# Optimization experiments

Hardware: AMD Instinct MI355X
Metric: run time of the kernel (lower is better)

The kernel has to match this reference:

```python
import jax, jax.numpy as jnp
import numpy as np
from jax import lax

EPS_BN = 1e-5
EPS_LN = 1e-5


def setup_inputs() -> dict:
    key = jax.random.key(0)
    ks = jax.random.split(key, 10)
    B, Cin, H, W = 32, 512, 56, 56
    Cout, Cr = 128, 128 // 16  # CBAM reduction 16
    x = jax.random.normal(ks[0], (B, Cin, H, W), dtype=jnp.float32)
    w_proj = jax.random.normal(ks[1], (Cout, Cin), dtype=jnp.float32) * 0.02
    bn_g = jnp.ones((Cout,), jnp.float32)
    bn_b = jnp.zeros((Cout,), jnp.float32)
    bn_m = jax.random.normal(ks[2], (Cout,), dtype=jnp.float32) * 0.1
    bn_v = jax.random.uniform(ks[3], (Cout,), dtype=jnp.float32, minval=0.5, maxval=1.5)
    ca_w1 = jax.random.normal(ks[4], (Cr, Cout), dtype=jnp.float32) * 0.05
    ca_w2 = jax.random.normal(ks[5], (Cout, Cr), dtype=jnp.float32) * 0.05
    sa_w = jax.random.normal(ks[6], (1, 2, 7, 7), dtype=jnp.float32) * 0.05
    ln_g = jnp.ones((Cout,), jnp.float32)
    ln_b = jnp.zeros((Cout,), jnp.float32)
    return dict(x=x, w_proj=w_proj, bn_g=bn_g, bn_b=bn_b, bn_m=bn_m, bn_v=bn_v,
                ca_w1=ca_w1, ca_w2=ca_w2, sa_w=sa_w, ln_g=ln_g, ln_b=ln_b)


def _cbam(x, ca_w1, ca_w2, sa_w):
    # Channel attention: shared MLP on GAP and GMP over spatial dims
    avg = x.mean(axis=(2, 3))  # [B, C]
    mx = x.max(axis=(2, 3))    # [B, C]
    mlp = lambda p: jnp.einsum('cr,br->bc', ca_w2, jax.nn.relu(jnp.einsum('rc,bc->br', ca_w1, p)))
    ca = jax.nn.sigmoid(mlp(avg) + mlp(mx))  # [B, C]
    x = x * ca[:, :, None, None]
    # Spatial attention: channel-wise avg/max -> 7x7 conv -> sigmoid
    s = jnp.stack([x.mean(axis=1), x.max(axis=1)], axis=1)  # [B, 2, H, W]
    sa = lax.conv_general_dilated(s, sa_w, (1, 1), [(3, 3), (3, 3)],
                                  dimension_numbers=('NCHW', 'OIHW', 'NCHW'))
    return x * jax.nn.sigmoid(sa)


def reference(x, w_proj, bn_g, bn_b, bn_m, bn_v, ca_w1, ca_w2, sa_w, ln_g, ln_b):
    # 1x1 conv (no bias) as GEMM over channels
    h = jnp.einsum('bchw,oc->bohw', x, w_proj)
    # BatchNorm (inference) + SiLU
    scale = (bn_g / jnp.sqrt(bn_v + EPS_BN))[None, :, None, None]
    shift = (bn_b - bn_m * bn_g / jnp.sqrt(bn_v + EPS_BN))[None, :, None, None]
    h = h * scale + shift
    h = h * jax.nn.sigmoid(h)  # SiLU
    # CBAM with residual
    y = _cbam(h, ca_w1, ca_w2, sa_w) + h
    # GAP over spatial -> LayerNorm over channels
    y = y.mean(axis=(2, 3))  # [B, C]
    mu = y.mean(axis=-1, keepdims=True)
    var = ((y - mu) ** 2).mean(axis=-1, keepdims=True)
    return (y - mu) / jnp.sqrt(var + EPS_LN) * ln_g + ln_b
```

## Files before the change

### kernel.cpp

```cpp
#include <hip/hip_runtime.h>
#include <hip/hip_bf16.h>

typedef __bf16 bf16x8 __attribute__((ext_vector_type(8)));
typedef float f32x4 __attribute__((ext_vector_type(4)));

#define NB 32
#define CIN 512
#define COUT 128
#define NP 3136
#define WIMG 56

__device__ __forceinline__ unsigned fenc(float f) {
    unsigned u = __float_as_uint(f);
    return (u & 0x80000000u) ? ~u : (u | 0x80000000u);
}
__device__ __forceinline__ float fdec(unsigned e) {
    unsigned u = (e & 0x80000000u) ? (e ^ 0x80000000u) : ~e;
    return __uint_as_float(u);
}
__device__ __forceinline__ float bflo(unsigned u) { return __uint_as_float(u << 16); }
__device__ __forceinline__ float bfhi(unsigned u) { return __uint_as_float(u & 0xffff0000u); }

__device__ __forceinline__ unsigned cvt2_fp8(float a, float b) {
    unsigned r;
    asm volatile("v_cvt_pk_fp8_f32 %0, %1, %2" : "=&v"(r) : "v"(a), "v"(b));
    return r & 0xffffu;
}
__device__ __forceinline__ unsigned pack4_fp8(unsigned u01, unsigned u23) {
    unsigned lo = cvt2_fp8(bflo(u01), bfhi(u01));
    unsigned hi = cvt2_fp8(bflo(u23), bfhi(u23));
    return lo | (hi << 16);
}
__device__ __forceinline__ unsigned pack4_fp8f(float a, float b, float c, float d) {
    return cvt2_fp8(a, b) | (cvt2_fp8(c, d) << 16);
}
__device__ __forceinline__ float fp8_entry(int v) {
    unsigned s = (v >> 7) & 1, e = (v >> 3) & 15, m = v & 7;
    if (e) return __uint_as_float((s << 31) | ((e + 120) << 23) | (m << 20));
    float f = (float)m * 0x1p-9f;
    return s ? -f : f;
}

__device__ __forceinline__ void lds_barrier() {
    asm volatile("s_waitcnt lgkmcnt(0)" ::: "memory");
    __builtin_amdgcn_s_barrier();
    __builtin_amdgcn_sched_barrier(0);
}

__global__ __launch_bounds__(256) void k_wcvt(const float* __restrict__ wp,
                                              unsigned* __restrict__ wf8,
                                              unsigned* __restrict__ zero8k)
{
    int i = blockIdx.x * 256 + threadIdx.x;
    if (i < 2 * NB * COUT) zero8k[i] = 0u;
    float4 f = *(const float4*)(wp + i * 4);
    wf8[i] = pack4_fp8f(f.x, f.y, f.z, f.w);
}

__global__ __launch_bounds__(512, 6) void k_main(
    const float* __restrict__ x, const uchar* __restrict__ wf8,
    const float* __restrict__ bn_g, const float* __restrict__ bn_b,
    const float* __restrict__ bn_m, const float* __restrict__ bn_v,
    uchar* __restrict__ hout, float* __restrict__ sumh, unsigned* __restrict__ mxenc)
{
    __shared__ __align__(16) uchar Xs[2][64 * 128];
    __shared__ __align__(16) uchar Ws[2][128 * 128];
    __shared__ float bnss[256];
    __shared__ float redS[2][COUT];
    __shared__ float redM[2][COUT];

    const int bid  = blockIdx.x;
    const int swz  = (bid & 7) * 196 + (bid >> 3);
    const int t    = threadIdx.x;
    const int b    = swz / 49;
    const int p0   = (swz % 49) * 64;
    const int lane = t & 63;
    const int l15  = lane & 15;
    const int lg   = lane >> 4;
    const int w    = t >> 6;
    const int wm   = w >> 1;
    const int wn   = w & 1;

    if (t < COUT) {
        float sc = bn_g[t] * rsqrtf(bn_v[t] + 1e-5f);
        bnss[t]        = sc;
        bnss[t + COUT] = bn_b[t] - bn_m[t] * sc;
    }

    const int pr = t & 63;
    const int kg = t >> 6;
    const float* xb = x + ((size_t)b * CIN) * NP + p0 + pr;
    const int xbyte = pr * 128 + ((kg * 16) ^ ((pr & 7) << 4));

    const int ow = t >> 2, kq = t & 3;
    const uchar* wsrc = wf8 + ow * CIN + kq * 32;
    const int wbyte0 = ow * 128 + ((kq * 32) ^ ((ow & 7) << 4));
    const int wbyte1 = ow * 128 + ((kq * 32 + 16) ^ ((ow & 7) << 4));

    f32x4 acc[2][2];
#pragma unroll
    for (int mf = 0; mf < 2; ++mf)
#pragma unroll
        for (int nf = 0; nf < 2; ++nf) acc[mf][nf] = (f32x4){0.f, 0.f, 0.f, 0.f};

    float ldx[2][16];
    uint4 ldw0, ldw1;

#pragma unroll
    for (int s = 0; s < 2; ++s)
#pragma unroll
        for (int j = 0; j < 16; ++j)
            ldx[s][j] = xb[(s * 128 + kg * 16 + j) * NP];
    ldw0 = *(const uint4*)(wsrc);
    ldw1 = *(const uint4*)(wsrc + 16);
    {
        uint4 v;
        v.x = pack4_fp8f(ldx[0][0],  ldx[0][1],  ldx[0][2],  ldx[0][3]);
        v.y = pack4_fp8f(ldx[0][4],  ldx[0][5],  ldx[0][6],  ldx[0][7]);
        v.z = pack4_fp8f(ldx[0][8],  ldx[0][9],  ldx[0][10], ldx[0][11]);
        v.w = pack4_fp8f(ldx[0][12], ldx[0][13], ldx[0][14], ldx[0][15]);
        *(uint4*)(Xs[0] + xbyte) = v;
        *(uint4*)(Ws[0] + wbyte0) = ldw0;
        *(uint4*)(Ws[0] + wbyte1) = ldw1;
    }

#pragma unroll
    for (int kc = 0; kc < 4; ++kc) {
        lds_barrier();
        if (kc < 2) {
#pragma unroll
            for (int j = 0; j < 16; ++j)
                ldx[kc & 1][j] = xb[((kc + 2) * 128 + kg * 16 + j) * NP];
        }
        if (kc < 3) {
            ldw0 = *(const uint4*)(wsrc + (kc + 1) * 128);
            ldw1 = *(const uint4*)(wsrc + (kc + 1) * 128 + 16);
        }
#pragma unroll
        for (int ks = 0; ks < 4; ++ks) {
            long af[2], bfr[2];
#pragma unroll
            for (int mf = 0; mf < 2; ++mf) {
                int o = wm * 32 + mf * 16 + l15;
                af[mf] = *(const long*)(Ws[kc & 1]
                          + o * 128 + ((ks * 32 + lg * 8) ^ ((o & 7) << 4)));
            }
#pragma unroll
            for (int nf = 0; nf < 2; ++nf) {
                int p = wn * 32 + nf * 16 + l15;
                bfr[nf] = *(const long*)(Xs[kc & 1]
                           + p * 128 + ((ks * 32 + lg * 8) ^ ((p & 7) << 4)));
            }
#pragma unroll
            for (int mf = 0; mf < 2; ++mf)
#pragma unroll
                for (int nf = 0; nf < 2; ++nf)
                    acc[mf][nf] = __builtin_amdgcn_mfma_f32_16x16x32_fp8_fp8(
                        af[mf], bfr[nf], acc[mf][nf], 0, 0, 0);
        }
        if (kc < 3) {
            uint4 v;
            const float* L = ldx[(kc + 1) & 1];
            v.x = pack4_fp8f(L[0],  L[1],  L[2],  L[3]);
            v.y = pack4_fp8f(L[4],  L[5],  L[6],  L[7]);
            v.z = pack4_fp8f(L[8],  L[9],  L[10], L[11]);
            v.w = pack4_fp8f(L[12], L[13], L[14], L[15]);
            *(uint4*)(Xs[(kc + 1) & 1] + xbyte) = v;
            *(uint4*)(Ws[(kc + 1) & 1] + wbyte0) = ldw0;
            *(uint4*)(Ws[(kc + 1) & 1] + wbyte1) = ldw1;
        }
    }

    __syncthreads();
    ushort* Hs = (ushort*)Xs;
#pragma unroll
    for (int mf = 0; mf < 2; ++mf) {
#pragma unroll
        for (int reg = 0; reg < 4; ++reg) {
            int o = wm * 32 + mf * 16 + lg * 4 + reg;
            float sc = bnss[o], sh = bnss[o + COUT];
            float s_ = 0.f, m_ = -1e30f;
#pragma unroll
            for (int nf = 0; nf < 2; ++nf) {
                float d    = acc[mf][nf][reg];
                float hval = d * sc + sh;
                hval       = hval / (1.f + __expf(-hval));
                s_ += hval;
                m_ = fmaxf(m_, hval);
                __bf16 hb = (__bf16)hval;
                Hs[o * 64 + wn * 32 + nf * 16 + l15] = *(ushort*)&hb;
            }
#pragma unroll
            for (int d = 1; d < 16; d <<= 1) {
                s_ += __shfl_xor(s_, d, 64);
                m_ = fmaxf(m_, __shfl_xor(m_, d, 64));
            }
            if (l15 == 0) {
                redS[wn][o] = s_;
                redM[wn][o] = m_;
            }
        }
    }
    __syncthreads();
    if (t < COUT) {
        atomicAdd(&sumh[b * COUT + t], redS[0][t] + redS[1][t]);
        atomicMax(&mxenc[b * COUT + t], fenc(fmaxf(redM[0][t], redM[1][t])));
    }
    {
        int orow = t >> 2, c = t & 3;
        uint4 a  = *(const uint4*)&Hs[orow * 64 + c * 16];
        uint4 b4 = *(const uint4*)&Hs[orow * 64 + c * 16 + 8];
        uint4 o4;
        o4.x = pack4_fp8(a.x, a.y);
        o4.y = pack4_fp8(a.z, a.w);
        o4.z = pack4_fp8(b4.x, b4.y);
        o4.w = pack4_fp8(b4.z, b4.w);
        *(uint4*)&hout[((size_t)b * COUT + orow) * NP + p0 + c * 16] = o4;
    }
}

__global__ __launch_bounds__(256) void k_sstat(const uchar* __restrict__ h,
                                               const float* __restrict__ sumh,
                                               const unsigned* __restrict__ mxenc,
                                               const float* __restrict__ w1,
                                               const float* __restrict__ w2,
                                               float* __restrict__ ca,
                                               float* __restrict__ sbuf)
{
    int b = blockIdx.y, z = blockIdx.z;
    int t = threadIdx.x;
    __shared__ float avg[128], mx[128], r1[16], cas[32], tab[256];
    tab[t] = fp8_entry(t);
    if (t < 128) {
        avg[t] = sumh[b * COUT + t] * (1.f / (float)NP);
        mx[t]  = fdec(mxenc[b * COUT + t]);
    }
    __syncthreads();
    if (t < 16) {
        int r = t & 7;
        const float* p = (t < 8) ? avg : mx;
        float s = 0.f;
        for (int c = 0; c < 128; ++c) s += w1[r * 128 + c] * p[c];
        r1[t] = fmaxf(s, 0.f);
    }
    __syncthreads();
    if (t < 32) {
        int o = z * 32 + t;
        float s = 0.f;
#pragma unroll
        for (int r = 0; r < 8; ++r) s += w2[o * 8 + r] * (r1[r] + r1[r + 8]);
        float cv = 1.f / (1.f + __expf(-s));
        cas[t] = cv;
        if (blockIdx.x == 0) ca[b * COUT + o] = cv;
    }
    __syncthreads();

    int idx = blockIdx.x * 256 + t;
    if (idx >= NP / 4) return;
    int p = idx * 4;
    const uchar* hb = h + ((size_t)(b * COUT + z * 32)) * NP + p;
    float s0 = 0.f, s1 = 0.f, s2 = 0.f, s3 = 0.f;
    float m0 = -1e30f, m1 = -1e30f, m2 = -1e30f, m3 = -1e30f;
#pragma unroll 4
    for (int c = 0; c < 32; ++c) {
        unsigned u = *(const unsigned*)(hb + (size_t)c * NP);
        float cv = cas[c];
        float v0 = tab[u & 255] * cv;
        float v1 = tab[(u >> 8) & 255] * cv;
        float v2 = tab[(u >> 16) & 255] * cv;
        float v3 = tab[u >> 24] * cv;
        s0 += v0; s1 += v1; s2 += v2; s3 += v3;
        m0 = fmaxf(m0, v0); m1 = fmaxf(m1, v1);
        m2 = fmaxf(m2, v2); m3 = fmaxf(m3, v3);
    }
    float* sb = sbuf + ((size_t)(z * NB + b) * 2) * NP;
    *(float4*)&sb[p]      = make_float4(s0, s1, s2, s3);
    *(float4*)&sb[NP + p] = make_float4(m0, m1, m2, m3);
}

__global__ __launch_bounds__(256) void k_conv(const float* __restrict__ sbuf,
                                              const float* __restrict__ saw,
                                              float* __restrict__ sigsa)
{
    int band = blockIdx.x, b = blockIdx.y;
    int y0 = band * 7;
    int t = threadIdx.x;
    __shared__ float s[2][13 * WIMG];
    __shared__ float w[98];
    if (t < 98) w[t] = saw[t];
    for (int i = t; i < 13 * WIMG; i += 256) {
        int yy = y0 - 3 + i / WIMG;
        float vs = 0.f, vm = 0.f;
        if (yy >= 0 && yy < WIMG) {
            int p = yy * WIMG + (i % WIMG);
            float ssum = 0.f, smax = -1e30f;
#pragma unroll
            for (int z = 0; z < 4; ++z) {
                const float* sb = sbuf + ((size_t)(z * NB + b) * 2) * NP;
                ssum += sb[p];
                smax = fmaxf(smax, sb[NP + p]);
            }
            vs = ssum * (1.f / (float)COUT);
            vm = smax;
        }
        s[0][i] = vs;
        s[1][i] = vm;
    }
    __syncthreads();
    for (int i = t; i < 7 * WIMG; i += 256) {
        int ly = i / WIMG, px = i % WIMG;
        float a = 0.f;
#pragma unroll
        for (int ch = 0; ch < 2; ++ch) {
#pragma unroll
            for (int dy = 0; dy < 7; ++dy) {
                int li = (ly + dy) * WIMG;
                for (int dx = 0; dx < 7; ++dx) {
                    int xx = px + dx - 3;
                    if (xx < 0 || xx >= WIMG) continue;
                    a += s[ch][li + xx] * w[ch * 49 + dy * 7 + dx];
                }
            }
        }
        sigsa[b * NP + (y0 + ly) * WIMG + px] = 1.f / (1.f + __expf(-a));
    }
}

__global__ __launch_bounds__(256) void k_wsum(const uchar* __restrict__ h,
                                              const float* __restrict__ sigsa,
                                              const float* __restrict__ sumh,
                                              const float* __restrict__ ca,
                                              float* __restrict__ y)
{
    int bo = blockIdx.x;
    int b = bo >> 7;
    int t = threadIdx.x;
    __shared__ float tab[256];
    __shared__ float part[4];
    tab[t] = fp8_entry(t);
    __syncthreads();
    const uchar* hr = h + (size_t)bo * NP;
    const float* sg  = sigsa + (size_t)b * NP;
    float s = 0.f;
#pragma unroll
    for (int i = 0; i < 3; ++i) {
        int q = i * 256 + t;
        unsigned u = *(const unsigned*)(hr + q * 4);
        float4 g = *(const float4*)(sg + q * 4);
        s += tab[u & 255] * g.x + tab[(u >> 8) & 255] * g.y
           + tab[(u >> 16) & 255] * g.z + tab[u >> 24] * g.w;
    }
    if (t < 16) {
        int q = 768 + t;
        unsigned u = *(const unsigned*)(hr + q * 4);
        float4 g = *(const float4*)(sg + q * 4);
        s += tab[u & 255] * g.x + tab[(u >> 8) & 255] * g.y
           + tab[(u >> 16) & 255] * g.z + tab[u >> 24] * g.w;
    }
#pragma unroll
    for (int d = 1; d < 64; d <<= 1) s += __shfl_xor(s, d, 64);
    if ((t & 63) == 0) part[t >> 6] = s;
    __syncthreads();
    if (t == 0) {
        float tt = part[0] + part[1] + part[2] + part[3];
        y[bo] = (sumh[bo] + ca[bo] * tt) * (1.f / (float)NP);
    }
}

__global__ void k_ln(const float* __restrict__ y, const float* __restrict__ g,
                     const float* __restrict__ bta, float* __restrict__ out)
{
    int b = blockIdx.x, t = threadIdx.x;
    __shared__ float pr[2], pr2[2];
    float v = y[b * COUT + t];
    float s = v;
#pragma unroll
    for (int d = 1; d < 64; d <<= 1) s += __shfl_xor(s, d, 64);
    if ((t & 63) == 0) pr[t >> 6] = s;
    __syncthreads();
    float mu = (pr[0] + pr[1]) * (1.f / (float)COUT);
    float dv = v - mu;
    float q = dv * dv;
#pragma unroll
    for (int d = 1; d < 64; d <<= 1) q += __shfl_xor(q, d, 64);
    if ((t & 63) == 0) pr2[t >> 6] = q;
    __syncthreads();
    float var = (pr2[0] + pr2[1]) * (1.f / (float)COUT);
    out[b * COUT + t] = dv * rsqrtf(var + 1e-5f) * g[t] + bta[t];
}

extern "C" void kernel_launch(void* const* d_in, const int* in_sizes, int n_in,
                              void* d_out, int out_size, void* d_ws, size_t ws_size,
                              hipStream_t stream)
{
    const float* x     = (const float*)d_in[0];
    const float* wp    = (const float*)d_in[1];
    const float* bn_g  = (const float*)d_in[2];
    const float* bn_b  = (const float*)d_in[3];
    const float* bn_m  = (const float*)d_in[4];
    const float* bn_v  = (const float*)d_in[5];
    const float* ca_w1 = (const float*)d_in[6];
    const float* ca_w2 = (const float*)d_in[7];
    const float* sa_w  = (const float*)d_in[8];
    const float* ln_g  = (const float*)d_in[9];
    const float* ln_b  = (const float*)d_in[10];
    float* out = (float*)d_out;

    char* ws = (char*)d_ws;
    size_t off = 0;
    uchar*    hbuf  = (uchar*)(ws + off);    off += (size_t)NB * COUT * NP;
    float*    sumh  = (float*)(ws + off);    off += NB * COUT * 4;
    unsigned* mxenc = (unsigned*)(ws + off); off += NB * COUT * 4;
    float*    ca    = (float*)(ws + off);    off += NB * COUT * 4;
    float*    sbuf  = (float*)(ws + off);    off += (size_t)4 * NB * 2 * NP * 4;
    float*    sigsa = (float*)(ws + off);    off += (size_t)NB * NP * 4;
    float*    ybuf  = (float*)(ws + off);    off += NB * COUT * 4;
    unsigned* wf8   = (unsigned*)(ws + off); off += (size_t)COUT * CIN;

    k_wcvt<<<64, 256, 0, stream>>>(wp, wf8, (unsigned*)sumh);
    k_main<<<NB * 49, 512, 0, stream>>>(x, (const uchar*)wf8, bn_g, bn_b, bn_m, bn_v,
                                        hbuf, sumh, mxenc);
    k_sstat<<<dim3(4, NB, 4), 256, 0, stream>>>(hbuf, sumh, mxenc, ca_w1, ca_w2, ca, sbuf);
    k_conv<<<dim3(8, NB), 256, 0, stream>>>(sbuf, sa_w, sigsa);
    k_wsum<<<NB * COUT, 256, 0, stream>>>(hbuf, sigsa, sumh, ca, ybuf);
    k_ln<<<NB, 128, 0, stream>>>(ybuf, ln_g, ln_b, out);
}
```

Measured before the change: 80.82 us.

## Process two pixel tiles per block with single-buffered LDS for higher occupancy

The main GEMM kernel now computes two consecutive 64-pixel tiles per block, launching 784 blocks instead of 1568. The LDS staging buffers drop from double to single buffering, and the epilogue reuses the weight buffer as the bf16 scratch area. Together these shrink shared memory per block, allowing the launch bound to rise from 6 to 8 blocks per SM so occupancy can go up. Prefetch into registers still overlaps the next chunk's global loads with MFMA work, including across the tile boundary. The cost is an extra barrier per K-chunk, since stores can no longer be hidden behind a second LDS buffer, plus possible register pressure under the tighter occupancy bound.

New measurement: 149.7 us. 85.2% more time.

```diff
diff --git a/kernel.cpp b/kernel.cpp
--- a/kernel.cpp
+++ b/kernel.cpp
@@ -57,23 +57,21 @@
     wf8[i] = pack4_fp8f(f.x, f.y, f.z, f.w);
 }
 
-__global__ __launch_bounds__(512, 6) void k_main(
+__global__ __launch_bounds__(512, 8) void k_main(
     const float* __restrict__ x, const uchar* __restrict__ wf8,
     const float* __restrict__ bn_g, const float* __restrict__ bn_b,
     const float* __restrict__ bn_m, const float* __restrict__ bn_v,
     uchar* __restrict__ hout, float* __restrict__ sumh, unsigned* __restrict__ mxenc)
 {
-    __shared__ __align__(16) uchar Xs[2][64 * 128];
-    __shared__ __align__(16) uchar Ws[2][128 * 128];
+    __shared__ __align__(16) uchar Xs[64 * 128];
+    __shared__ __align__(16) uchar Ws[128 * 128];
     __shared__ float bnss[256];
     __shared__ float redS[2][COUT];
     __shared__ float redM[2][COUT];
 
     const int bid  = blockIdx.x;
-    const int swz  = (bid & 7) * 196 + (bid >> 3);
+    const int swz  = (bid & 7) * 98 + (bid >> 3);
     const int t    = threadIdx.x;
-    const int b    = swz / 49;
-    const int p0   = (swz % 49) * 64;
     const int lane = t & 63;
     const int l15  = lane & 15;
     const int lg   = lane >> 4;
@@ -87,9 +85,15 @@
         bnss[t + COUT] = bn_b[t] - bn_m[t] * sc;
     }
 
+    const int s0 = swz * 2;
+    const int b0 = s0 / 49,      p00 = (s0 % 49) * 64;
+    const int s1 = s0 + 1;
+    const int b1 = s1 / 49,      p01 = (s1 % 49) * 64;
+
     const int pr = t & 63;
     const int kg = t >> 6;
-    const float* xb = x + ((size_t)b * CIN) * NP + p0 + pr;
+    const float* xb0 = x + ((size_t)b0 * CIN) * NP + p00 + pr;
+    const float* xb1 = x + ((size_t)b1 * CIN) * NP + p01 + pr;
     const int xbyte = pr * 128 + ((kg * 16) ^ ((pr & 7) << 4));
 
     const int ow = t >> 2, kq = t & 3;
@@ -97,125 +101,124 @@
     const int wbyte0 = ow * 128 + ((kq * 32) ^ ((ow & 7) << 4));
     const int wbyte1 = ow * 128 + ((kq * 32 + 16) ^ ((ow & 7) << 4));
 
-    f32x4 acc[2][2];
-#pragma unroll
-    for (int mf = 0; mf < 2; ++mf)
-#pragma unroll
-        for (int nf = 0; nf < 2; ++nf) acc[mf][nf] = (f32x4){0.f, 0.f, 0.f, 0.f};
-
-    float ldx[2][16];
+    float ldx[16];
     uint4 ldw0, ldw1;
 
 #pragma unroll
-    for (int s = 0; s < 2; ++s)
-#pragma unroll
-        for (int j = 0; j < 16; ++j)
-            ldx[s][j] = xb[(s * 128 + kg * 16 + j) * NP];
+    for (int j = 0; j < 16; ++j) ldx[j] = xb0[(kg * 16 + j) * NP];
     ldw0 = *(const uint4*)(wsrc);
     ldw1 = *(const uint4*)(wsrc + 16);
-    {
-        uint4 v;
-        v.x = pack4_fp8f(ldx[0][0],  ldx[0][1],  ldx[0][2],  ldx[0][3]);
-        v.y = pack4_fp8f(ldx[0][4],  ldx[0][5],  ldx[0][6],  ldx[0][7]);
-        v.z = pack4_fp8f(ldx[0][8],  ldx[0][9],  ldx[0][10], ldx[0][11]);
-        v.w = pack4_fp8f(ldx[0][12], ldx[0][13], ldx[0][14], ldx[0][15]);
-        *(uint4*)(Xs[0] + xbyte) = v;
-        *(uint4*)(Ws[0] + wbyte0) = ldw0;
-        *(uint4*)(Ws[0] + wbyte1) = ldw1;
-    }
-
-#pragma unroll
-    for (int kc = 0; kc < 4; ++kc) {
+
+#pragma unroll
+    for (int si = 0; si < 2; ++si) {
+        const int b_  = si ? b1 : b0;
+        const int p0_ = si ? p01 : p00;
+        const float* xbn = si ? xb0  : xb1;
+
+        f32x4 acc[2][2];
+#pragma unroll
+        for (int mf = 0; mf < 2; ++mf)
+#pragma unroll
+            for (int nf = 0; nf < 2; ++nf) acc[mf][nf] = (f32x4){0.f, 0.f, 0.f, 0.f};
+
+#pragma unroll
+        for (int kc = 0; kc < 4; ++kc) {
+            lds_barrier();
+            {
+                uint4 v;
+                v.x = pack4_fp8f(ldx[0],  ldx[1],  ldx[2],  ldx[3]);
+                v.y = pack4_fp8f(ldx[4],  ldx[5],  ldx[6],  ldx[7]);
+                v.z = pack4_fp8f(ldx[8],  ldx[9],  ldx[10], ldx[11]);
+                v.w = pack4_fp8f(ldx[12], ldx[13], ldx[14], ldx[15]);
+                *(uint4*)(Xs + xbyte) = v;
+                *(uint4*)(Ws + wbyte0) = ldw0;
+                *(uint4*)(Ws + wbyte1) = ldw1;
+            }
+            if (kc < 3) {
+                const float* xc = si ? xb1 : xb0;
+#pragma unroll
+                for (int j = 0; j < 16; ++j)
+                    ldx[j] = xc[((kc + 1) * 128 + kg * 16 + j) * NP];
+                ldw0 = *(const uint4*)(wsrc + (kc + 1) * 128);
+                ldw1 = *(const uint4*)(wsrc + (kc + 1) * 128 + 16);
+            } else if (si == 0) {
+#pragma unroll
+                for (int j = 0; j < 16; ++j)
+                    ldx[j] = xbn[(kg * 16 + j) * NP];
+                ldw0 = *(const uint4*)(wsrc);
+                ldw1 = *(const uint4*)(wsrc + 16);
+            }
+            lds_barrier();
+#pragma unroll
+            for (int ks = 0; ks < 4; ++ks) {
+                long af[2], bfr[2];
+#pragma unroll
+                for (int mf = 0; mf < 2; ++mf) {
+                    int o = wm * 32 + mf * 16 + l15;
+                    af[mf] = *(const long*)(Ws
+                              + o * 128 + ((ks * 32 + lg * 8) ^ ((o & 7) << 4)));
+                }
+#pragma unroll
+                for (int nf = 0; nf < 2; ++nf) {
+                    int p = wn * 32 + nf * 16 + l15;
+                    bfr[nf] = *(const long*)(Xs
+                               + p * 128 + ((ks * 32 + lg * 8) ^ ((p & 7) << 4)));
+                }
+#pragma unroll
+                for (int mf = 0; mf < 2; ++mf)
+#pragma unroll
+                    for (int nf = 0; nf < 2; ++nf)
+                        acc[mf][nf] = __builtin_amdgcn_mfma_f32_16x16x32_fp8_fp8(
+                            af[mf], bfr[nf], acc[mf][nf], 0, 0, 0);
+            }
+        }
+
         lds_barrier();
-        if (kc < 2) {
-#pragma unroll
-            for (int j = 0; j < 16; ++j)
-                ldx[kc & 1][j] = xb[((kc + 2) * 128 + kg * 16 + j) * NP];
-        }
-        if (kc < 3) {
-            ldw0 = *(const uint4*)(wsrc + (kc + 1) * 128);
-            ldw1 = *(const uint4*)(wsrc + (kc + 1) * 128 + 16);
-        }
-#pragma unroll
-        for (int ks = 0; ks < 4; ++ks) {
-            long af[2], bfr[2];
-#pragma unroll
-            for (int mf = 0; mf < 2; ++mf) {
-                int o = wm * 32 + mf * 16 + l15;
-                af[mf] = *(const long*)(Ws[kc & 1]
-                          + o * 128 + ((ks * 32 + lg * 8) ^ ((o & 7) << 4)));
-            }
-#pragma unroll
-            for (int nf = 0; nf < 2; ++nf) {
-                int p = wn * 32 + nf * 16 + l15;
-                bfr[nf] = *(const long*)(Xs[kc & 1]
-                           + p * 128 + ((ks * 32 + lg * 8) ^ ((p & 7) << 4)));
-            }
-#pragma unroll
-            for (int mf = 0; mf < 2; ++mf)
-#pragma unroll
-                for (int nf = 0; nf < 2; ++nf)
-                    acc[mf][nf] = __builtin_amdgcn_mfma_f32_16x16x32_fp8_fp8(
-                        af[mf], bfr[nf], acc[mf][nf], 0, 0, 0);
-        }
-        if (kc < 3) {
-            uint4 v;
-            const float* L = ldx[(kc + 1) & 1];
-            v.x = pack4_fp8f(L[0],  L[1],  L[2],  L[3]);
-            v.y = pack4_fp8f(L[4],  L[5],  L[6],  L[7]);
-            v.z = pack4_fp8f(L[8],  L[9],  L[10], L[11]);
-            v.w = pack4_fp8f(L[12], L[13], L[14], L[15]);
-            *(uint4*)(Xs[(kc + 1) & 1] + xbyte) = v;
-            *(uint4*)(Ws[(kc + 1) & 1] + wbyte0) = ldw0;
-            *(uint4*)(Ws[(kc + 1) & 1] + wbyte1) = ldw1;
-        }
-    }
-
-    __syncthreads();
-    ushort* Hs = (ushort*)Xs;
-#pragma unroll
-    for (int mf = 0; mf < 2; ++mf) {
-#pragma unroll
-        for (int reg = 0; reg < 4; ++reg) {
-            int o = wm * 32 + mf * 16 + lg * 4 + reg;
-            float sc = bnss[o], sh = bnss[o + COUT];
-            float s_ = 0.f, m_ = -1e30f;
-#pragma unroll
-            for (int nf = 0; nf < 2; ++nf) {
-                float d    = acc[mf][nf][reg];
-                float hval = d * sc + sh;
-                hval       = hval / (1.f + __expf(-hval));
-                s_ += hval;
-                m_ = fmaxf(m_, hval);
-                __bf16 hb = (__bf16)hval;
-                Hs[o * 64 + wn * 32 + nf * 16 + l15] = *(ushort*)&hb;
-            }
-#pragma unroll
-            for (int d = 1; d < 16; d <<= 1) {
-                s_ += __shfl_xor(s_, d, 64);
-                m_ = fmaxf(m_, __shfl_xor(m_, d, 64));
-            }
-            if (l15 == 0) {
-                redS[wn][o] = s_;
-                redM[wn][o] = m_;
-            }
-        }
-    }
-    __syncthreads();
-    if (t < COUT) {
-        atomicAdd(&sumh[b * COUT + t], redS[0][t] + redS[1][t]);
-        atomicMax(&mxenc[b * COUT + t], fenc(fmaxf(redM[0][t], redM[1][t])));
-    }
-    {
-        int orow = t >> 2, c = t & 3;
-        uint4 a  = *(const uint4*)&Hs[orow * 64 + c * 16];
-        uint4 b4 = *(const uint4*)&Hs[orow * 64 + c * 16 + 8];
-        uint4 o4;
-        o4.x = pack4_fp8(a.x, a.y);
-        o4.y = pack4_fp8(a.z, a.w);
-        o4.z = pack4_fp8(b4.x, b4.y);
-        o4.w = pack4_fp8(b4.z, b4.w);
-        *(uint4*)&hout[((size_t)b * COUT + orow) * NP + p0 + c * 16] = o4;
+        ushort* Hs = (ushort*)Ws;
+#pragma unroll
+        for (int mf = 0; mf < 2; ++mf) {
+#pragma unroll
+            for (int reg = 0; reg < 4; ++reg) {
+                int o = wm * 32 + mf * 16 + lg * 4 + reg;
+                float sc = bnss[o], sh = bnss[o + COUT];
+                float s_ = 0.f, m_ = -1e30f;
+#pragma unroll
+                for (int nf = 0; nf < 2; ++nf) {
+                    float d    = acc[mf][nf][reg];
+                    float hval = d * sc + sh;
+                    hval       = hval / (1.f + __expf(-hval));
+                    s_ += hval;
+                    m_ = fmaxf(m_, hval);
+                    __bf16 hb = (__bf16)hval;
+                    Hs[o * 64 + wn * 32 + nf * 16 + l15] = *(ushort*)&hb;
+                }
+#pragma unroll
+                for (int d = 1; d < 16; d <<= 1) {
+                    s_ += __shfl_xor(s_, d, 64);
+                    m_ = fmaxf(m_, __shfl_xor(m_, d, 64));
+                }
+                if (l15 == 0) {
+                    redS[wn][o] = s_;
+                    redM[wn][o] = m_;
+                }
+            }
+        }
+        lds_barrier();
+        if (t < COUT) {
+            atomicAdd(&sumh[b_ * COUT + t], redS[0][t] + redS[1][t]);
+            atomicMax(&mxenc[b_ * COUT + t], fenc(fmaxf(redM[0][t], redM[1][t])));
+        }
+        {
+            int orow = t >> 2, c = t & 3;
+            uint4 a  = *(const uint4*)&Hs[orow * 64 + c * 16];
+            uint4 b4 = *(const uint4*)&Hs[orow * 64 + c * 16 + 8];
+            uint4 o4;
+            o4.x = pack4_fp8(a.x, a.y);
+            o4.y = pack4_fp8(a.z, a.w);
+            o4.z = pack4_fp8(b4.x, b4.y);
+            o4.w = pack4_fp8(b4.z, b4.w);
+            *(uint4*)&hout[((size_t)b_ * COUT + orow) * NP + p0_ + c * 16] = o4;
+        }
     }
 }
 
@@ -418,8 +421,8 @@
     unsigned* wf8   = (unsigned*)(ws + off); off += (size_t)COUT * CIN;
 
     k_wcvt<<<64, 256, 0, stream>>>(wp, wf8, (unsigned*)sumh);
-    k_main<<<NB * 49, 512, 0, stream>>>(x, (const uchar*)wf8, bn_g, bn_b, bn_m, bn_v,
-                                        hbuf, sumh, mxenc);
+    k_main<<<784, 512, 0, stream>>>(x, (const uchar*)wf8, bn_g, bn_b, bn_m, bn_v,
+                                    hbuf, sumh, mxenc);
     k_sstat<<<dim3(4, NB, 4), 256, 0, stream>>>(hbuf, sumh, mxenc, ca_w1, ca_w2, ca, sbuf);
     k_conv<<<dim3(8, NB), 256, 0, stream>>>(sbuf, sa_w, sigsa);
     k_wsum<<<NB * COUT, 256, 0, stream>>>(hbuf, sigsa, sumh, ca, ybuf);
```
